# Kernel optimization log

Measured on AMD Instinct MI355X. Metric: run time of the kernel, lower is better.

## Reference

```python
import jax, jax.numpy as jnp
import numpy as np

EPS = 1e-7

def _sample_project(feat, pid, w1, b1, w2, b2):
    # feat: [B, C, H, W]; pid: [P] flat spatial indices into H*W
    B, C, H, W = feat.shape
    fr = jnp.transpose(feat, (0, 2, 3, 1)).reshape(B, H * W, C)  # [B, HW, C]
    x = fr[:, pid, :].reshape(B * pid.shape[0], C)               # gather -> [B*P, C]
    x = jnp.maximum(x @ w1 + b1, 0.0) @ w2 + b2                  # 2-layer MLP
    norm = jnp.sqrt(jnp.sum(x * x, axis=1, keepdims=True))       # L2 over channels
    return x / (norm + EPS)


def setup_inputs() -> dict:
    key = jax.random.key(0)
    ks = jax.random.split(key, 16)
    NC = 256
    shapes = [(16, 256, 128, 128), (16, 512, 64, 64), (16, 1024, 32, 32)]
    inp = {}
    for i, s in enumerate(shapes):
        inp[f"feat{i}"] = jax.random.normal(ks[i], s, dtype=jnp.float32)
        hw = s[2] * s[3]
        inp[f"patch_id{i}"] = jax.random.randint(ks[3 + i], (256,), 0, hw, dtype=jnp.int64)
        C = s[1]
        g = 0.02  # init_gain (normal init)
        inp[f"w1_{i}"] = g * jax.random.normal(ks[6 + 3 * i], (C, NC), dtype=jnp.float32)
        inp[f"b1_{i}"] = jnp.zeros((NC,), dtype=jnp.float32)
        inp[f"w2_{i}"] = g * jax.random.normal(ks[7 + 3 * i], (NC, NC), dtype=jnp.float32)
        inp[f"b2_{i}"] = jnp.zeros((NC,), dtype=jnp.float32)
    return inp


def reference(feat0, feat1, feat2, patch_id0, patch_id1, patch_id2,
              w1_0, b1_0, w2_0, b2_0,
              w1_1, b1_1, w2_1, b2_1,
              w1_2, b1_2, w2_2, b2_2):
    out0 = _sample_project(feat0, patch_id0, w1_0, b1_0, w2_0, b2_0)
    out1 = _sample_project(feat1, patch_id1, w1_1, b1_1, w2_1, b2_1)
    out2 = _sample_project(feat2, patch_id2, w1_2, b1_2, w2_2, b2_2)
    return (out0, out1, out2)
```

## Files before the change

kernel.cpp:

```cpp
#include <hip/hip_runtime.h>

typedef __attribute__((ext_vector_type(8))) short short8;
typedef __attribute__((ext_vector_type(4))) float floatx4;
typedef __attribute__((ext_vector_type(4))) unsigned int uintx4;

__device__ __forceinline__ short f2bf(float f) {
    unsigned u = __builtin_bit_cast(unsigned, f);
    u = (u + 0x7FFFu + ((u >> 16) & 1u)) >> 16;
    return (short)u;
}

__global__ __launch_bounds__(256) void prep_w(
    const float* __restrict__ w10, const float* __restrict__ w11, const float* __restrict__ w12,
    const float* __restrict__ w20, const float* __restrict__ w21, const float* __restrict__ w22,
    unsigned short* __restrict__ wsb)
{
    __shared__ float tile[32][33];
    int blk = blockIdx.x;
    const float* in; unsigned short* out; int K, t0;
    if (blk < 64)       { in = w10; out = wsb;          K = 256;  t0 = 0; }
    else if (blk < 192) { in = w11; out = wsb + 65536;  K = 512;  t0 = 64; }
    else if (blk < 448) { in = w12; out = wsb + 196608; K = 1024; t0 = 192; }
    else if (blk < 512) { in = w20; out = wsb + 458752; K = 256;  t0 = 448; }
    else if (blk < 576) { in = w21; out = wsb + 524288; K = 256;  t0 = 512; }
    else                { in = w22; out = wsb + 589824; K = 256;  t0 = 576; }
    int tile_id = blk - t0;
    int tk = K >> 5;
    int k0 = (tile_id % tk) << 5;
    int n0 = (tile_id / tk) << 5;
    int t = threadIdx.x;
    int j = t & 31, i0 = (t >> 5) << 2;
    #pragma unroll
    for (int u = 0; u < 4; u++)
        tile[i0 + u][j] = in[(size_t)(k0 + i0 + u) * 256 + (n0 + j)];
    __syncthreads();
    int kf = t & 31, nf0 = (t >> 5) << 2;
    #pragma unroll
    for (int u = 0; u < 4; u++)
        out[(size_t)(n0 + nf0 + u) * K + (k0 + kf)] = (unsigned short)f2bf(tile[kf][nf0 + u]);
}

__global__ __launch_bounds__(256, 2) void fused_mlp(
    const float* __restrict__ feat0, const float* __restrict__ feat1, const float* __restrict__ feat2,
    const int* __restrict__ pid0, const int* __restrict__ pid1, const int* __restrict__ pid2,
    const float* __restrict__ b1_0, const float* __restrict__ b1_1, const float* __restrict__ b1_2,
    const float* __restrict__ b2_0, const float* __restrict__ b2_1, const float* __restrict__ b2_2,
    const unsigned short* __restrict__ wsb,
    float* __restrict__ out)
{
    __shared__ __align__(16) unsigned short smem[26944];
    unsigned short* wsS = smem;
    unsigned short* xs  = smem + 18432;
    unsigned short* hs  = smem + 18432;
    float* rs = (float*)(smem + 26880);

    int blk = blockIdx.x;
    int scale = 2 - (blk >> 7);
    int mblk = blk & 127;

    const float* feat; const int* pid; const float* b1; const float* b2;
    const unsigned short* w1T; const unsigned short* w2T;
    int C, HW; size_t outBase;
    if (scale == 0) { feat = feat0; pid = pid0; b1 = b1_0; b2 = b2_0;
                      w1T = wsb;          w2T = wsb + 458752; C = 256;  HW = 16384; outBase = 0; }
    else if (scale == 1) { feat = feat1; pid = pid1; b1 = b1_1; b2 = b2_1;
                      w1T = wsb + 65536;  w2T = wsb + 524288; C = 512;  HW = 4096;  outBase = 1048576; }
    else            { feat = feat2; pid = pid2; b1 = b1_2; b2 = b2_2;
                      w1T = wsb + 196608; w2T = wsb + 589824; C = 1024; HW = 1024;  outBase = 2097152; }

    int t = threadIdx.x;
    int wid = t >> 6, lane = t & 63, quad = lane >> 4, l15 = lane & 15;
    int r0 = (wid & 1) << 4;
    int c0 = (wid >> 1) << 7;

    int gr = t >> 3;
    int gk = (t & 7) << 3;
    int row_g = (mblk << 5) + gr;
    int bb = row_g >> 8, pp = row_g & 255;
    int s = pid[pp];
    const float* fbase = feat + (size_t)bb * ((size_t)C * HW) + s;

    floatx4 acc[8];
    #pragma unroll
    for (int f = 0; f < 8; f++) acc[f] = (floatx4){0.f, 0.f, 0.f, 0.f};

    for (int kc = 0; kc < C; kc += 64) {
        {
            const float* gp = fbase + (size_t)(kc + gk) * HW;
            float v[8];
            #pragma unroll
            for (int j2 = 0; j2 < 8; j2++) v[j2] = gp[(size_t)j2 * HW];
            short8 sv;
            #pragma unroll
            for (int j2 = 0; j2 < 8; j2++) sv[j2] = f2bf(v[j2]);
            *(short8*)(xs + gr * 72 + gk) = sv;
        }
        {
            const uintx4* src = (const uintx4*)(w1T + (size_t)t * C + kc);
            uintx4* dst = (uintx4*)(wsS + t * 72);
            #pragma unroll
            for (int j2 = 0; j2 < 8; j2++) dst[j2] = src[j2];
        }
        __syncthreads();
        const unsigned short* aRow = xs + (r0 + l15) * 72;
        const unsigned short* bRow = wsS + (c0 + l15) * 72;
        #pragma unroll
        for (int ks = 0; ks < 2; ks++) {
            short8 af = *(const short8*)(aRow + ks * 32 + quad * 8);
            #pragma unroll
            for (int f = 0; f < 8; f++) {
                short8 bf = *(const short8*)(bRow + f * (16 * 72) + ks * 32 + quad * 8);
                acc[f] = __builtin_amdgcn_mfma_f32_16x16x32_bf16(af, bf, acc[f], 0, 0, 0);
            }
        }
        __syncthreads();
    }

    {
        float bias1[8];
        #pragma unroll
        for (int f = 0; f < 8; f++) bias1[f] = b1[c0 + f * 16 + l15];
        #pragma unroll
        for (int f = 0; f < 8; f++)
            #pragma unroll
            for (int reg = 0; reg < 4; reg++) {
                float h = fmaxf(acc[f][reg] + bias1[f], 0.f);
                hs[(r0 + quad * 4 + reg) * 264 + (c0 + f * 16 + l15)] = (unsigned short)f2bf(h);
            }
    }

    #pragma unroll
    for (int f = 0; f < 8; f++) acc[f] = (floatx4){0.f, 0.f, 0.f, 0.f};
    const unsigned short* hA = hs + (r0 + l15) * 264;
    for (int kc = 0; kc < 256; kc += 64) {
        {
            const uintx4* src = (const uintx4*)(w2T + (size_t)t * 256 + kc);
            uintx4* dst = (uintx4*)(wsS + t * 72);
            #pragma unroll
            for (int j2 = 0; j2 < 8; j2++) dst[j2] = src[j2];
        }
        __syncthreads();
        const unsigned short* bRow = wsS + (c0 + l15) * 72;
        #pragma unroll
        for (int ks = 0; ks < 2; ks++) {
            short8 af = *(const short8*)(hA + kc + ks * 32 + quad * 8);
            #pragma unroll
            for (int f = 0; f < 8; f++) {
                short8 bf = *(const short8*)(bRow + f * (16 * 72) + ks * 32 + quad * 8);
                acc[f] = __builtin_amdgcn_mfma_f32_16x16x32_bf16(af, bf, acc[f], 0, 0, 0);
            }
        }
        __syncthreads();
    }

    {
        float bias2[8];
        #pragma unroll
        for (int f = 0; f < 8; f++) bias2[f] = b2[c0 + f * 16 + l15];
        float psq[4] = {0.f, 0.f, 0.f, 0.f};
        #pragma unroll
        for (int f = 0; f < 8; f++)
            #pragma unroll
            for (int reg = 0; reg < 4; reg++) {
                float yv = acc[f][reg] + bias2[f];
                acc[f][reg] = yv;
                psq[reg] += yv * yv;
            }
        #pragma unroll
        for (int m = 1; m < 16; m <<= 1)
            #pragma unroll
            for (int reg = 0; reg < 4; reg++)
                psq[reg] += __shfl_xor(psq[reg], m, 16);

        if (t < 32) rs[t] = 0.f;
        __syncthreads();
        if (l15 == 0) {
            #pragma unroll
            for (int reg = 0; reg < 4; reg++)
                atomicAdd(&rs[r0 + quad * 4 + reg], psq[reg]);
        }
        __syncthreads();

        #pragma unroll
        for (int f = 0; f < 8; f++)
            #pragma unroll
            for (int reg = 0; reg < 4; reg++) {
                int row = r0 + quad * 4 + reg;
                float inv = 1.f / (sqrtf(rs[row]) + 1e-7f);
                out[outBase + (size_t)((mblk << 5) + row) * 256 + (c0 + f * 16 + l15)] =
                    acc[f][reg] * inv;
            }
    }
}

extern "C" void kernel_launch(void* const* d_in, const int* in_sizes, int n_in,
                              void* d_out, int out_size, void* d_ws, size_t ws_size,
                              hipStream_t stream)
{
    (void)n_in; (void)out_size; (void)ws_size;
    bool dict = (in_sizes[1] == 256);
    const float *feat[3], *w1[3], *b1[3], *w2[3], *b2[3];
    const int* pid[3];
    for (int i = 0; i < 3; i++) {
        if (dict) {
            feat[i] = (const float*)d_in[i * 6 + 0];
            pid[i]  = (const int*)  d_in[i * 6 + 1];
            w1[i]   = (const float*)d_in[i * 6 + 2];
            b1[i]   = (const float*)d_in[i * 6 + 3];
            w2[i]   = (const float*)d_in[i * 6 + 4];
            b2[i]   = (const float*)d_in[i * 6 + 5];
        } else {
            feat[i] = (const float*)d_in[i];
            pid[i]  = (const int*)  d_in[3 + i];
            w1[i]   = (const float*)d_in[6 + 4 * i + 0];
            b1[i]   = (const float*)d_in[6 + 4 * i + 1];
            w2[i]   = (const float*)d_in[6 + 4 * i + 2];
            b2[i]   = (const float*)d_in[6 + 4 * i + 3];
        }
    }
    unsigned short* wsb = (unsigned short*)d_ws;
    prep_w<<<640, 256, 0, stream>>>(w1[0], w1[1], w1[2], w2[0], w2[1], w2[2], wsb);
    fused_mlp<<<384, 256, 0, stream>>>(feat[0], feat[1], feat[2],
                                       pid[0], pid[1], pid[2],
                                       b1[0], b1[1], b1[2],
                                       b2[0], b2[1], b2[2],
                                       wsb, (float*)d_out);
}
```

Measured before the change: 542.4 us.

## Split strided feature gather into separate high-parallelism kernel before MLP

Moves the strided gather and bf16 conversion of sampled feature columns out of the fused MLP kernel into a dedicated gather_x kernel with 3584 blocks. The gathered rows are written to workspace in row-major bf16, and the MLP kernel then reads its A fragments straight from global memory instead of staging them in LDS. The aim is to expose far more memory-level parallelism for the latency-bound scattered reads than the 384-block fused kernel had. In exchange it adds an extra launch, a round trip of the gathered data through global memory, and uncached per-lane global loads inside the MFMA loop. The launch-bounds occupancy hint of 2 blocks per CU on the MLP kernel is also dropped.

```diff
diff --git a/kernel.cpp b/kernel.cpp
--- a/kernel.cpp
+++ b/kernel.cpp
@@ -9,6 +9,7 @@
     u = (u + 0x7FFFu + ((u >> 16) & 1u)) >> 16;
     return (short)u;
 }
+
 
 __global__ __launch_bounds__(256) void prep_w(
     const float* __restrict__ w10, const float* __restrict__ w11, const float* __restrict__ w12,
@@ -40,9 +41,34 @@
         out[(size_t)(n0 + nf0 + u) * K + (k0 + kf)] = (unsigned short)f2bf(tile[kf][nf0 + u]);
 }
 
-__global__ __launch_bounds__(256, 2) void fused_mlp(
-    const float* __restrict__ feat0, const float* __restrict__ feat1, const float* __restrict__ feat2,
-    const int* __restrict__ pid0, const int* __restrict__ pid1, const int* __restrict__ pid2,
+__global__ __launch_bounds__(256) void gather_x(
+    const float* __restrict__ f0, const float* __restrict__ f1, const float* __restrict__ f2,
+    const int* __restrict__ p0, const int* __restrict__ p1, const int* __restrict__ p2,
+    unsigned short* __restrict__ xg)
+{
+    int blk = blockIdx.x;
+    const float* feat; const int* pid; int C, HW, sh; unsigned short* dst;
+    if (blk < 512)        { feat = f0; pid = p0; C = 256;  HW = 16384; sh = 5; dst = xg; }
+    else if (blk < 1536)  { feat = f1; pid = p1; C = 512;  HW = 4096;  sh = 6; dst = xg + 1048576; blk -= 512; }
+    else                  { feat = f2; pid = p2; C = 1024; HW = 1024;  sh = 7; dst = xg + 3145728; blk -= 1536; }
+
+    int q   = (blk << 8) + threadIdx.x;
+    int row = q >> sh;
+    int c0  = (q & ((1 << sh) - 1)) << 3;
+    int b   = row >> 8, pp = row & 255;
+    int s   = pid[pp];
+    const float* src = feat + ((size_t)b * C + c0) * HW + s;
+
+    float v[8];
+    #pragma unroll
+    for (int j = 0; j < 8; j++) v[j] = src[(size_t)j * HW];
+    short8 sv;
+    #pragma unroll
+    for (int j = 0; j < 8; j++) sv[j] = f2bf(v[j]);
+    *(short8*)(dst + (size_t)row * C + c0) = sv;
+}
+
+__global__ __launch_bounds__(256) void mlp(
     const float* __restrict__ b1_0, const float* __restrict__ b1_1, const float* __restrict__ b1_2,
     const float* __restrict__ b2_0, const float* __restrict__ b2_1, const float* __restrict__ b2_2,
     const unsigned short* __restrict__ wsb,
@@ -50,7 +76,6 @@
 {
     __shared__ __align__(16) unsigned short smem[26944];
     unsigned short* wsS = smem;
-    unsigned short* xs  = smem + 18432;
     unsigned short* hs  = smem + 18432;
     float* rs = (float*)(smem + 26880);
 
@@ -58,43 +83,28 @@
     int scale = 2 - (blk >> 7);
     int mblk = blk & 127;
 
-    const float* feat; const int* pid; const float* b1; const float* b2;
-    const unsigned short* w1T; const unsigned short* w2T;
-    int C, HW; size_t outBase;
-    if (scale == 0) { feat = feat0; pid = pid0; b1 = b1_0; b2 = b2_0;
-                      w1T = wsb;          w2T = wsb + 458752; C = 256;  HW = 16384; outBase = 0; }
-    else if (scale == 1) { feat = feat1; pid = pid1; b1 = b1_1; b2 = b2_1;
-                      w1T = wsb + 65536;  w2T = wsb + 524288; C = 512;  HW = 4096;  outBase = 1048576; }
-    else            { feat = feat2; pid = pid2; b1 = b1_2; b2 = b2_2;
-                      w1T = wsb + 196608; w2T = wsb + 589824; C = 1024; HW = 1024;  outBase = 2097152; }
+    const float* b1; const float* b2;
+    const unsigned short* w1T; const unsigned short* w2T; const unsigned short* xg;
+    int C; size_t outBase;
+    if (scale == 0)      { b1 = b1_0; b2 = b2_0; w1T = wsb;          w2T = wsb + 458752;
+                           xg = wsb + 655360;           C = 256;  outBase = 0; }
+    else if (scale == 1) { b1 = b1_1; b2 = b2_1; w1T = wsb + 65536;  w2T = wsb + 524288;
+                           xg = wsb + 655360 + 1048576; C = 512;  outBase = 1048576; }
+    else                 { b1 = b1_2; b2 = b2_2; w1T = wsb + 196608; w2T = wsb + 589824;
+                           xg = wsb + 655360 + 3145728; C = 1024; outBase = 2097152; }
 
     int t = threadIdx.x;
     int wid = t >> 6, lane = t & 63, quad = lane >> 4, l15 = lane & 15;
     int r0 = (wid & 1) << 4;
     int c0 = (wid >> 1) << 7;
 
-    int gr = t >> 3;
-    int gk = (t & 7) << 3;
-    int row_g = (mblk << 5) + gr;
-    int bb = row_g >> 8, pp = row_g & 255;
-    int s = pid[pp];
-    const float* fbase = feat + (size_t)bb * ((size_t)C * HW) + s;
-
     floatx4 acc[8];
     #pragma unroll
     for (int f = 0; f < 8; f++) acc[f] = (floatx4){0.f, 0.f, 0.f, 0.f};
 
+    const unsigned short* aG = xg + (size_t)((mblk << 5) + r0 + l15) * C;
+
     for (int kc = 0; kc < C; kc += 64) {
-        {
-            const float* gp = fbase + (size_t)(kc + gk) * HW;
-            float v[8];
-            #pragma unroll
-            for (int j2 = 0; j2 < 8; j2++) v[j2] = gp[(size_t)j2 * HW];
-            short8 sv;
-            #pragma unroll
-            for (int j2 = 0; j2 < 8; j2++) sv[j2] = f2bf(v[j2]);
-            *(short8*)(xs + gr * 72 + gk) = sv;
-        }
         {
             const uintx4* src = (const uintx4*)(w1T + (size_t)t * C + kc);
             uintx4* dst = (uintx4*)(wsS + t * 72);
@@ -102,11 +112,10 @@
             for (int j2 = 0; j2 < 8; j2++) dst[j2] = src[j2];
         }
         __syncthreads();
-        const unsigned short* aRow = xs + (r0 + l15) * 72;
         const unsigned short* bRow = wsS + (c0 + l15) * 72;
         #pragma unroll
         for (int ks = 0; ks < 2; ks++) {
-            short8 af = *(const short8*)(aRow + ks * 32 + quad * 8);
+            short8 af = *(const short8*)(aG + kc + ks * 32 + quad * 8);
             #pragma unroll
             for (int f = 0; f < 8; f++) {
                 short8 bf = *(const short8*)(bRow + f * (16 * 72) + ks * 32 + quad * 8);
@@ -219,10 +228,11 @@
         }
     }
     unsigned short* wsb = (unsigned short*)d_ws;
+    gather_x<<<3584, 256, 0, stream>>>(feat[0], feat[1], feat[2],
+                                       pid[0], pid[1], pid[2],
+                                       wsb + 655360);
     prep_w<<<640, 256, 0, stream>>>(w1[0], w1[1], w1[2], w2[0], w2[1], w2[2], wsb);
-    fused_mlp<<<384, 256, 0, stream>>>(feat[0], feat[1], feat[2],
-                                       pid[0], pid[1], pid[2],
-                                       b1[0], b1[1], b1[2],
-                                       b2[0], b2[1], b2[2],
-                                       wsb, (float*)d_out);
-}
+    mlp<<<384, 256, 0, stream>>>(b1[0], b1[1], b1[2],
+                                 b2[0], b2[1], b2[2],
+                                 wsb, (float*)d_out);
+}
```

After: 561.4 us. 1.04x slower.
